# Optimization experiments

Measured on AMD Instinct MI355X. Metric: run time of the kernel, lower is better.

The kernel has to match this reference:

```python
import jax, jax.numpy as jnp
import numpy as np

# --- quantization helpers (I-BERT-style symmetric quantization) ---

def _quant_int(x, scale, bit):
    # round(x/scale) clamped to signed `bit`-bit range (SymmetricQuantFunction)
    n = 2 ** (bit - 1) - 1
    return jnp.clip(jnp.round(x / scale), -n - 1, n)


def quant_linear(x, s_x, W, b, weight_bit=8):
    """QuantLinear: per-output-channel symmetric 8-bit weight quant, int GEMM, dequant.
    Returns (output, bias_scaling_factor[out_features])."""
    n = 2 ** (weight_bit - 1) - 1
    w_scale = jnp.maximum(jnp.max(jnp.abs(W), axis=1), 1e-8) / n          # (out,)
    w_int = _quant_int(W, w_scale[:, None], weight_bit)                   # int-valued (out,in)
    b_scale = w_scale * s_x                                               # (out,) broadcasts with scalar s_x
    b_int = jnp.round(b / b_scale)                                        # 32-bit bias, no clamp needed
    x_int = x / s_x                                                       # int-valued activations
    out_int = jnp.einsum('bsi,oi->bso', x_int, w_int) + b_int
    return out_int * b_scale, b_scale


def quant_act(x, bit):
    """QuantAct: per-tensor symmetric requantization to `bit` bits (dynamic min/max)."""
    n = 2 ** (bit - 1) - 1
    scale = jnp.maximum(jnp.max(jnp.abs(x)), 1e-8) / n                    # scalar
    x_int = _quant_int(x, scale, bit)
    return x_int * scale, scale


def int_gelu(x, s):
    """IntGELU (I-BERT): integer 2nd-order polynomial approximation of erf."""
    k = 1.4142
    c0, c1 = -0.2888, -1.769
    c2 = 1.0 / c0
    SHIFT = 14  # 'const' in the original code

    x_int = x / s
    se = s / k  # scaling factor fed to int_erf
    # --- int_erf ---
    b_int = jnp.floor(c1 / se)
    c_int = jnp.floor(c2 / se ** 2)
    sign = jnp.sign(x_int)
    abs_int = jnp.minimum(jnp.abs(x_int), -b_int)
    y_int = sign * ((abs_int + b_int) ** 2 + c_int)
    se2 = se ** 2 * c0
    y_int = jnp.floor(y_int / 2 ** SHIFT)
    se2 = se2 * 2 ** SHIFT
    # --- gelu = x * (erf/2 + 1/2) in integer form ---
    shift_int = jnp.floor(1.0 / se2)
    out_int = x_int * (y_int + shift_int)
    s_out = s * se2 / 2
    return out_int * s_out, s_out


def setup_inputs() -> dict:
    key = jax.random.key(0)
    k_x, k_w1, k_b1, k_w2, k_b2 = jax.random.split(key, 5)
    B, S, D, H = 8, 1024, 768, 3072
    x = jax.random.normal(k_x, (B, S, D), dtype=jnp.float32)
    act_scaling_factor = jnp.full((1,), 0.02, dtype=jnp.float32)
    # pre-quantize x onto its input grid (x arrives already quantized in the real pipeline)
    x = jnp.round(x / act_scaling_factor) * act_scaling_factor
    W1 = jax.random.normal(k_w1, (H, D), dtype=jnp.float32) * 0.02
    b1 = jax.random.normal(k_b1, (H,), dtype=jnp.float32) * 0.02
    W2 = jax.random.normal(k_w2, (D, H), dtype=jnp.float32) * 0.02
    b2 = jax.random.normal(k_b2, (D,), dtype=jnp.float32) * 0.02
    return {"x": x, "act_scaling_factor": act_scaling_factor,
            "W1": W1, "b1": b1, "W2": W2, "b2": b2}


def reference(x, act_scaling_factor, W1, b1, W2, b2):
    s = act_scaling_factor
    h, s = quant_linear(x, s, W1, b1)       # fc1: int8 GEMM + dequant
    h, s = quant_act(h, 8)                  # qact_gelu
    h, s = int_gelu(h, s)                   # IntGELU
    h, s = quant_act(h, 8)                  # qact1 (drop=0.0 -> identity)
    h, s = quant_linear(h, s, W2, b2)       # fc2
    h, s = quant_act(h, 16)                 # qact2 (16-bit)
    return h, s
```

## Files before the change

kernel.cpp:

```cpp
#include <hip/hip_runtime.h>

typedef _Float16 half8  __attribute__((ext_vector_type(8)));
typedef _Float16 half4v __attribute__((ext_vector_type(4)));
typedef float f32x4 __attribute__((ext_vector_type(4)));
typedef int int4v __attribute__((ext_vector_type(4)));

#define M_DIM 8192
#define D_DIM 768
#define H_DIM 3072

#define WS_WSCALE2   16
#define WS_BINT1     (WS_WSCALE2 + 768*4)
#define WS_BSCALE1   (WS_BINT1 + 3072*4)
#define WS_BINT2     (WS_BSCALE1 + 3072*4)
#define WS_BSCALE2   (WS_BINT2 + 768*4)
#define WS_XQ        34560UL
#define WS_WQ1       (WS_XQ  + (size_t)M_DIM*D_DIM*2)
#define WS_WQ2I      (WS_WQ1 + (size_t)H_DIM*D_DIM*2)
#define WS_H1        (WS_WQ2I + (size_t)D_DIM*H_DIM)
#define WS_Q2        WS_H1
#define WS_H2        (WS_H1 + (size_t)M_DIM*H_DIM)
#define WS_Q1        (WS_H1 + (size_t)M_DIM*H_DIM*4)

__device__ __forceinline__ void gl_lds16(const _Float16* g, _Float16* l) {
  __builtin_amdgcn_global_load_lds(
      (const __attribute__((address_space(1))) void*)g,
      (__attribute__((address_space(3))) void*)l, 16, 0, 0);
}
__device__ __forceinline__ void gl_lds16c(const char* g, char* l) {
  __builtin_amdgcn_global_load_lds(
      (const __attribute__((address_space(1))) void*)g,
      (__attribute__((address_space(3))) void*)l, 16, 0, 0);
}

struct GeluP { float scale1, bintg, cintg, shiftint, s_out; };

__device__ __forceinline__ GeluP gelu_params(float max1) {
  GeluP p;
  p.scale1 = fmaxf(max1, 1e-8f) / 127.0f;
  float se = p.scale1 / 1.4142f;
  p.bintg = floorf(-1.769f / se);
  p.cintg = floorf(((float)(1.0 / -0.2888)) / (se * se));
  float se2 = ((se * se) * -0.2888f) * 16384.0f;
  p.shiftint = floorf(1.0f / se2);
  p.s_out = (p.scale1 * se2) * 0.5f;
  return p;
}

__device__ __forceinline__ float gelu_val(const GeluP& p, float qf) {
  float sg = (qf > 0.f) ? 1.f : ((qf < 0.f) ? -1.f : 0.f);
  float aq = fminf(fabsf(qf), -p.bintg);
  float t = aq + p.bintg;
  float y = sg * (t * t + p.cintg);
  float yf = floorf(y * (1.0f / 16384.0f));
  return (qf * (yf + p.shiftint)) * p.s_out;
}

__global__ __launch_bounds__(256)
void k1_prep(const float* __restrict__ W1, const float* __restrict__ b1,
             const float* __restrict__ W2, const float* __restrict__ sxp,
             _Float16* __restrict__ wq1, char* __restrict__ wq2i,
             float* __restrict__ wscale2, float* __restrict__ bint1,
             float* __restrict__ bscale1, unsigned* __restrict__ wsu)
{
  if (blockIdx.x == 0 && threadIdx.x == 0) { wsu[0] = 0u; wsu[1] = 0u; wsu[2] = 0u; }
  int w = blockIdx.x * 4 + (threadIdx.x >> 6);
  int lane = threadIdx.x & 63;
  if (w < H_DIM) {
    const float* row = W1 + (size_t)w * D_DIM;
    f32x4 v[3]; float m = 0.f;
#pragma unroll
    for (int t = 0; t < 3; t++) {
      v[t] = *(const f32x4*)(row + t * 256 + lane * 4);
#pragma unroll
      for (int j = 0; j < 4; j++) m = fmaxf(m, fabsf(v[t][j]));
    }
#pragma unroll
    for (int off = 32; off >= 1; off >>= 1) m = fmaxf(m, __shfl_xor(m, off));
    float wsc = fmaxf(m, 1e-8f) / 127.0f;
    _Float16* orow = wq1 + (size_t)w * D_DIM;
#pragma unroll
    for (int t = 0; t < 3; t++) {
      half4v h;
#pragma unroll
      for (int j = 0; j < 4; j++) {
        float q = fminf(fmaxf(rintf(v[t][j] / wsc), -128.f), 127.f);
        h[j] = (_Float16)q;
      }
      *(half4v*)(orow + t * 256 + lane * 4) = h;
    }
    if (lane == 0) {
      float bs = wsc * sxp[0];
      bint1[w] = rintf(b1[w] / bs);
      bscale1[w] = bs;
    }
  } else {
    int o = w - H_DIM;
    const float* row = W2 + (size_t)o * H_DIM;
    f32x4 v[12]; float m = 0.f;
#pragma unroll
    for (int t = 0; t < 12; t++) {
      v[t] = *(const f32x4*)(row + t * 256 + lane * 4);
#pragma unroll
      for (int j = 0; j < 4; j++) m = fmaxf(m, fabsf(v[t][j]));
    }
#pragma unroll
    for (int off = 32; off >= 1; off >>= 1) m = fmaxf(m, __shfl_xor(m, off));
    float wsc = fmaxf(m, 1e-8f) / 127.0f;
    unsigned* orow = (unsigned*)(wq2i + (size_t)o * H_DIM);
#pragma unroll
    for (int t = 0; t < 12; t++) {
      unsigned pk = 0;
#pragma unroll
      for (int j = 0; j < 4; j++) {
        float q = fminf(fmaxf(rintf(v[t][j] / wsc), -128.f), 127.f);
        pk |= ((unsigned)(unsigned char)(char)(int)q) << (8 * j);
      }
      orow[t * 64 + lane] = pk;
    }
    if (lane == 0) wscale2[o] = wsc;
  }
}

__global__ __launch_bounds__(256)
void k2_quant_x(const float* __restrict__ x, const float* __restrict__ sxp,
                _Float16* __restrict__ xq, int n4)
{
  float sx = sxp[0];
  int stride = gridDim.x * blockDim.x;
  for (int i = blockIdx.x * blockDim.x + threadIdx.x; i < n4; i += stride) {
    f32x4 v = ((const f32x4*)x)[i];
    half4v h;
#pragma unroll
    for (int j = 0; j < 4; j++) h[j] = (_Float16)(v[j] / sx);
    ((half4v*)xq)[i] = h;
  }
}

#define F16_SLOT 8192

__global__ __launch_bounds__(256)
void gemm_f16_dp(const _Float16* __restrict__ A, const _Float16* __restrict__ B,
                 const float* __restrict__ bint, const float* __restrict__ bscale,
                 float* __restrict__ C, unsigned* __restrict__ maxw, int N, int K)
{
  __shared__ _Float16 lds[3 * F16_SLOT];
  __shared__ float wred[4];
  const int tid = threadIdx.x;
  const int wid = tid >> 6;
  const int lane = tid & 63;
  const int m0 = blockIdx.x * 128;
  const int n0 = blockIdx.y * 128;
  const int wm = wid >> 1;
  const int wn = wid & 1;

  const int sr = tid >> 2;
  const int sc = tid & 3;
  const int csw = sc ^ ((sr >> 1) & 3);
  const _Float16* pa0 = A + (size_t)(m0 + sr) * K + csw * 8;
  const _Float16* pa1 = A + (size_t)(m0 + 64 + sr) * K + csw * 8;
  const _Float16* pb0 = B + (size_t)(n0 + sr) * K + csw * 8;
  const _Float16* pb1 = B + (size_t)(n0 + 64 + sr) * K + csw * 8;

#define STAGE_F(t, s) do {                                                   \
    _Float16* const base = lds + (s) * F16_SLOT + wid * 512;                 \
    gl_lds16(pa0 + (size_t)(t) * 32, base);                                  \
    gl_lds16(pa1 + (size_t)(t) * 32, base + 2048);                           \
    gl_lds16(pb0 + (size_t)(t) * 32, base + 4096);                           \
    gl_lds16(pb1 + (size_t)(t) * 32, base + 6144);                           \
  } while (0)

  int aoff[4], boff[4];
  const int ks = lane >> 4;
#pragma unroll
  for (int f = 0; f < 4; f++) {
    int r = wm * 64 + f * 16 + (lane & 15);
    aoff[f] = r * 64 + ((ks ^ ((r >> 1) & 3)) * 16);
    int rn = wn * 64 + f * 16 + (lane & 15);
    boff[f] = 8192 + rn * 64 + ((ks ^ ((rn >> 1) & 3)) * 16);
  }

  f32x4 acc[4][4];
#pragma unroll
  for (int i = 0; i < 4; i++)
#pragma unroll
    for (int j = 0; j < 4; j++) acc[i][j] = (f32x4){0.f, 0.f, 0.f, 0.f};

  const int nt = K / 32;
  STAGE_F(0, 0);
  STAGE_F(1, 1);
  for (int t = 0; t < nt; ++t) {
    const int s = t % 3;
    if (t + 1 < nt) asm volatile("s_waitcnt vmcnt(4)" ::: "memory");
    else            asm volatile("s_waitcnt vmcnt(0)" ::: "memory");
    asm volatile("s_barrier" ::: "memory");
    if (t + 2 < nt) STAGE_F(t + 2, (t + 2) % 3);
    const char* sb = (const char*)(lds + s * F16_SLOT);
    half8 a[4], b01[2], b23[2];
#pragma unroll
    for (int f = 0; f < 4; f++) a[f] = *(const half8*)(sb + aoff[f]);
    b01[0] = *(const half8*)(sb + boff[0]);
    b01[1] = *(const half8*)(sb + boff[1]);
    __builtin_amdgcn_s_setprio(1);
#pragma unroll
    for (int i = 0; i < 4; i++)
#pragma unroll
      for (int j = 0; j < 2; j++)
        acc[i][j] = __builtin_amdgcn_mfma_f32_16x16x32_f16(a[i], b01[j], acc[i][j], 0, 0, 0);
    __builtin_amdgcn_s_setprio(0);
    b23[0] = *(const half8*)(sb + boff[2]);
    b23[1] = *(const half8*)(sb + boff[3]);
    __builtin_amdgcn_s_setprio(1);
#pragma unroll
    for (int i = 0; i < 4; i++)
#pragma unroll
      for (int j = 0; j < 2; j++)
        acc[i][j + 2] = __builtin_amdgcn_mfma_f32_16x16x32_f16(a[i], b23[j], acc[i][j + 2], 0, 0, 0);
    __builtin_amdgcn_s_setprio(0);
  }
#undef STAGE_F

  float tmax = 0.f;
  const int orow0 = m0 + wm * 64 + (lane >> 4) * 4;
  const int ocol0 = n0 + wn * 64 + (lane & 15);
#pragma unroll
  for (int j = 0; j < 4; j++) {
    const int col = ocol0 + j * 16;
    const float bi = bint[col];
    const float bs = bscale[col];
#pragma unroll
    for (int i = 0; i < 4; i++) {
#pragma unroll
      for (int e = 0; e < 4; e++) {
        const int rowm = orow0 + i * 16 + e;
        float v = (acc[i][j][e] + bi) * bs;
        C[(size_t)rowm * N + col] = v;
        tmax = fmaxf(tmax, fabsf(v));
      }
    }
  }
#pragma unroll
  for (int off = 32; off >= 1; off >>= 1) tmax = fmaxf(tmax, __shfl_xor(tmax, off));
  if (lane == 0) wred[wid] = tmax;
  __syncthreads();
  if (tid == 0) {
    float bm = fmaxf(fmaxf(wred[0], wred[1]), fmaxf(wred[2], wred[3]));
    atomicMax(maxw, __float_as_uint(bm));
  }
}

__global__ __launch_bounds__(256)
void k4_gelu(const float* __restrict__ h1, const unsigned* __restrict__ wsu,
             char* __restrict__ q1, unsigned* __restrict__ maxw, int n4)
{
  GeluP p = gelu_params(__uint_as_float(wsu[0]));
  float tmax = 0.f;
  int stride = gridDim.x * blockDim.x;
  for (int i = blockIdx.x * blockDim.x + threadIdx.x; i < n4; i += stride) {
    f32x4 h = ((const f32x4*)h1)[i];
    unsigned pack = 0;
#pragma unroll
    for (int j = 0; j < 4; j++) {
      float qf = fminf(fmaxf(rintf(h[j] / p.scale1), -128.f), 127.f);
      tmax = fmaxf(tmax, fabsf(gelu_val(p, qf)));
      pack |= ((unsigned)(unsigned char)(char)(int)qf) << (8 * j);
    }
    ((unsigned*)q1)[i] = pack;
  }
#pragma unroll
  for (int off = 32; off >= 1; off >>= 1) tmax = fmaxf(tmax, __shfl_xor(tmax, off));
  __shared__ float wred[4];
  int wid = threadIdx.x >> 6;
  if ((threadIdx.x & 63) == 0) wred[wid] = tmax;
  __syncthreads();
  if (threadIdx.x == 0) {
    float bm = fmaxf(fmaxf(wred[0], wred[1]), fmaxf(wred[2], wred[3]));
    atomicMax(maxw, __float_as_uint(bm));
  }
}

__global__ __launch_bounds__(256)
void k6_bias(const unsigned* __restrict__ wsu, const float* __restrict__ wscale2,
             const float* __restrict__ b2, float* __restrict__ bint2,
             float* __restrict__ bscale2)
{
  float scale2 = fmaxf(__uint_as_float(wsu[1]), 1e-8f) / 127.0f;
  for (int o = threadIdx.x; o < D_DIM; o += 256) {
    float bs = wscale2[o] * scale2;
    bint2[o] = rintf(b2[o] / bs);
    bscale2[o] = bs;
  }
}

__global__ __launch_bounds__(256)
void k5_q2(const char* __restrict__ q1, const unsigned* __restrict__ wsu,
           char* __restrict__ q2, int n16)
{
  GeluP p = gelu_params(__uint_as_float(wsu[0]));
  float scale2 = fmaxf(__uint_as_float(wsu[1]), 1e-8f) / 127.0f;
  int stride = gridDim.x * blockDim.x;
  for (int i = blockIdx.x * blockDim.x + threadIdx.x; i < n16; i += stride) {
    uint4 pk = ((const uint4*)q1)[i];
    uint4 o;
    unsigned* pw[4] = {&o.x, &o.y, &o.z, &o.w};
    unsigned pr[4] = {pk.x, pk.y, pk.z, pk.w};
#pragma unroll
    for (int w = 0; w < 4; w++) {
      unsigned acc = 0;
#pragma unroll
      for (int j = 0; j < 4; j++) {
        float qf = (float)(int)(signed char)(pr[w] >> (8 * j));
        float g = gelu_val(p, qf);
        float q2f = fminf(fmaxf(rintf(g / scale2), -128.f), 127.f);
        acc |= ((unsigned)(unsigned char)(char)(int)q2f) << (8 * j);
      }
      *pw[w] = acc;
    }
    ((uint4*)q2)[i] = o;
  }
}

#define I8_SLOT 12288

__global__ __launch_bounds__(256)
void gemm_i8_dp(const char* __restrict__ A, const char* __restrict__ B,
                const float* __restrict__ bint, const float* __restrict__ bscale,
                float* __restrict__ C, unsigned* __restrict__ maxw, int N, int K)
{
  __shared__ char lds[3 * I8_SLOT];
  __shared__ float wred[4];
  const int tid = threadIdx.x;
  const int wid = tid >> 6;
  const int lane = tid & 63;
  const int m0 = blockIdx.x * 64;
  const int n0 = blockIdx.y * 128;
  const int wm = wid >> 1;
  const int wn = wid & 1;

  const int sr = tid >> 2;
  const int sc = tid & 3;
  const int csw = sc ^ ((sr >> 1) & 3);
  const char* pa  = A + (size_t)(m0 + sr) * K + csw * 16;
  const char* pb0 = B + (size_t)(n0 + sr) * K + csw * 16;
  const char* pb1 = B + (size_t)(n0 + 64 + sr) * K + csw * 16;

#define STAGE_I(t, s) do {                                                   \
    char* const base = lds + (s) * I8_SLOT + wid * 1024;                     \
    gl_lds16c(pa  + (size_t)(t) * 64, base);                                 \
    gl_lds16c(pb0 + (size_t)(t) * 64, base + 4096);                          \
    gl_lds16c(pb1 + (size_t)(t) * 64, base + 8192);                          \
  } while (0)

  int aoff[2], boff[4];
  const int ks = lane >> 4;
#pragma unroll
  for (int f = 0; f < 2; f++) {
    int r = wm * 32 + f * 16 + (lane & 15);
    aoff[f] = r * 64 + ((ks ^ ((r >> 1) & 3)) * 16);
  }
#pragma unroll
  for (int f = 0; f < 4; f++) {
    int rn = wn * 64 + f * 16 + (lane & 15);
    boff[f] = 4096 + rn * 64 + ((ks ^ ((rn >> 1) & 3)) * 16);
  }

  int4v acc[2][4];
#pragma unroll
  for (int i = 0; i < 2; i++)
#pragma unroll
    for (int j = 0; j < 4; j++) acc[i][j] = (int4v){0, 0, 0, 0};

  const int nt = K / 64;
  STAGE_I(0, 0);
  STAGE_I(1, 1);
  for (int t = 0; t < nt; ++t) {
    const int s = t % 3;
    if (t + 1 < nt) asm volatile("s_waitcnt vmcnt(3)" ::: "memory");
    else            asm volatile("s_waitcnt vmcnt(0)" ::: "memory");
    asm volatile("s_barrier" ::: "memory");
    if (t + 2 < nt) STAGE_I(t + 2, (t + 2) % 3);
    const char* sb = lds + s * I8_SLOT;
    int4v a[2], b01[2], b23[2];
#pragma unroll
    for (int f = 0; f < 2; f++) a[f] = *(const int4v*)(sb + aoff[f]);
    b01[0] = *(const int4v*)(sb + boff[0]);
    b01[1] = *(const int4v*)(sb + boff[1]);
    __builtin_amdgcn_s_setprio(1);
#pragma unroll
    for (int i = 0; i < 2; i++)
#pragma unroll
      for (int j = 0; j < 2; j++)
        acc[i][j] = __builtin_amdgcn_mfma_i32_16x16x64_i8(a[i], b01[j], acc[i][j], 0, 0, 0);
    __builtin_amdgcn_s_setprio(0);
    b23[0] = *(const int4v*)(sb + boff[2]);
    b23[1] = *(const int4v*)(sb + boff[3]);
    __builtin_amdgcn_s_setprio(1);
#pragma unroll
    for (int i = 0; i < 2; i++)
#pragma unroll
      for (int j = 0; j < 2; j++)
        acc[i][j + 2] = __builtin_amdgcn_mfma_i32_16x16x64_i8(a[i], b23[j], acc[i][j + 2], 0, 0, 0);
    __builtin_amdgcn_s_setprio(0);
  }
#undef STAGE_I

  float tmax = 0.f;
  const int orow0 = m0 + wm * 32 + (lane >> 4) * 4;
  const int ocol0 = n0 + wn * 64 + (lane & 15);
#pragma unroll
  for (int j = 0; j < 4; j++) {
    const int col = ocol0 + j * 16;
    const float bi = bint[col];
    const float bs = bscale[col];
#pragma unroll
    for (int i = 0; i < 2; i++) {
#pragma unroll
      for (int e = 0; e < 4; e++) {
        const int rowm = orow0 + i * 16 + e;
        float v = ((float)acc[i][j][e] + bi) * bs;
        C[(size_t)rowm * N + col] = v;
        tmax = fmaxf(tmax, fabsf(v));
      }
    }
  }
#pragma unroll
  for (int off = 32; off >= 1; off >>= 1) tmax = fmaxf(tmax, __shfl_xor(tmax, off));
  if (lane == 0) wred[wid] = tmax;
  __syncthreads();
  if (tid == 0) {
    float bm = fmaxf(fmaxf(wred[0], wred[1]), fmaxf(wred[2], wred[3]));
    atomicMax(maxw, __float_as_uint(bm));
  }
}

__global__ __launch_bounds__(256)
void k7_final(const float* __restrict__ h2, const unsigned* __restrict__ wsu,
              float* __restrict__ out, int n4, int ntot)
{
  float scale16 = fmaxf(__uint_as_float(wsu[2]), 1e-8f) / 32767.0f;
  int stride = gridDim.x * blockDim.x;
  for (int i = blockIdx.x * blockDim.x + threadIdx.x; i < n4; i += stride) {
    f32x4 v = ((const f32x4*)h2)[i];
    f32x4 o;
#pragma unroll
    for (int j = 0; j < 4; j++) {
      float q = fminf(fmaxf(rintf(v[j] / scale16), -32768.f), 32767.f);
      o[j] = q * scale16;
    }
    ((f32x4*)out)[i] = o;
  }
  if (blockIdx.x == 0 && threadIdx.x == 0) out[ntot] = scale16;
}

extern "C" void kernel_launch(void* const* d_in, const int* in_sizes, int n_in,
                              void* d_out, int out_size, void* d_ws, size_t ws_size,
                              hipStream_t stream)
{
  (void)in_sizes; (void)n_in; (void)out_size; (void)ws_size;
  const float* x  = (const float*)d_in[0];
  const float* sx = (const float*)d_in[1];
  const float* W1 = (const float*)d_in[2];
  const float* b1 = (const float*)d_in[3];
  const float* W2 = (const float*)d_in[4];
  const float* b2 = (const float*)d_in[5];
  float* out = (float*)d_out;
  char* ws = (char*)d_ws;

  unsigned* wsu   = (unsigned*)ws;
  float* wscale2  = (float*)(ws + WS_WSCALE2);
  float* bint1    = (float*)(ws + WS_BINT1);
  float* bscale1  = (float*)(ws + WS_BSCALE1);
  float* bint2    = (float*)(ws + WS_BINT2);
  float* bscale2  = (float*)(ws + WS_BSCALE2);
  _Float16* xq    = (_Float16*)(ws + WS_XQ);
  _Float16* wq1   = (_Float16*)(ws + WS_WQ1);
  char* wq2i      = (char*)(ws + WS_WQ2I);
  float* h1       = (float*)(ws + WS_H1);
  char* q2        = (char*)(ws + WS_Q2);
  float* h2       = (float*)(ws + WS_H2);
  char* q1        = (char*)(ws + WS_Q1);

  k1_prep<<<dim3(960), dim3(256), 0, stream>>>(W1, b1, W2, sx, wq1, wq2i, wscale2, bint1, bscale1, wsu);
  k2_quant_x<<<dim3(2048), dim3(256), 0, stream>>>(x, sx, xq, (M_DIM * D_DIM) / 4);
  gemm_f16_dp<<<dim3(64, 24), dim3(256), 0, stream>>>(xq, wq1, bint1, bscale1, h1, wsu + 0, H_DIM, D_DIM);
  k4_gelu<<<dim3(2048), dim3(256), 0, stream>>>(h1, wsu, q1, wsu + 1, (M_DIM * H_DIM) / 4);
  k6_bias<<<dim3(1), dim3(256), 0, stream>>>(wsu, wscale2, b2, bint2, bscale2);
  k5_q2<<<dim3(2048), dim3(256), 0, stream>>>(q1, wsu, q2, (M_DIM * H_DIM) / 16);
  gemm_i8_dp<<<dim3(128, 6), dim3(256), 0, stream>>>(q2, wq2i, bint2, bscale2, h2, wsu + 2, D_DIM, H_DIM);
  k7_final<<<dim3(2048), dim3(256), 0, stream>>>(h2, wsu, out, (M_DIM * D_DIM) / 4, M_DIM * D_DIM);
}
```

Before: 196.1 us.

## Rewrite fc1 GEMM as 256x256 8-phase pipeline and fuse prep kernels

The fc1 fp16 GEMM moves from 128x128 tiles with 4 waves and a 3-slot ring to 256x256 tiles with 8 waves. It uses a double-buffered 128 KB LDS layout with K=64 stages and an eight-phase schedule that interleaves global-to-LDS loads with MFMA groups. The goal is more data reuse per tile and better overlap of loads with math. Separately, the x-quantization kernel is merged into the weight-prep kernel, and the single-block fc2 bias kernel is folded into the int8 GEMM epilogue, which removes two launches. The large tile halves the grid and needs a lot of LDS and registers, so occupancy and tail effects are a risk.

```diff
diff --git a/kernel.cpp b/kernel.cpp
--- a/kernel.cpp
+++ b/kernel.cpp
@@ -12,8 +12,6 @@
 #define WS_WSCALE2   16
 #define WS_BINT1     (WS_WSCALE2 + 768*4)
 #define WS_BSCALE1   (WS_BINT1 + 3072*4)
-#define WS_BINT2     (WS_BSCALE1 + 3072*4)
-#define WS_BSCALE2   (WS_BINT2 + 768*4)
 #define WS_XQ        34560UL
 #define WS_WQ1       (WS_XQ  + (size_t)M_DIM*D_DIM*2)
 #define WS_WQ2I      (WS_WQ1 + (size_t)H_DIM*D_DIM*2)
@@ -31,6 +29,10 @@
   __builtin_amdgcn_global_load_lds(
       (const __attribute__((address_space(1))) void*)g,
       (__attribute__((address_space(3))) void*)l, 16, 0, 0);
+}
+__device__ __forceinline__ void vmw4or0(bool four) {
+  if (four) asm volatile("s_waitcnt vmcnt(4)" ::: "memory");
+  else      asm volatile("s_waitcnt vmcnt(0)" ::: "memory");
 }
 
 struct GeluP { float scale1, bintg, cintg, shiftint, s_out; };
@@ -57,183 +59,193 @@
 }
 
 __global__ __launch_bounds__(256)
-void k1_prep(const float* __restrict__ W1, const float* __restrict__ b1,
-             const float* __restrict__ W2, const float* __restrict__ sxp,
-             _Float16* __restrict__ wq1, char* __restrict__ wq2i,
-             float* __restrict__ wscale2, float* __restrict__ bint1,
-             float* __restrict__ bscale1, unsigned* __restrict__ wsu)
+void k12_prep(const float* __restrict__ W1, const float* __restrict__ b1,
+              const float* __restrict__ W2, const float* __restrict__ x,
+              const float* __restrict__ sxp,
+              _Float16* __restrict__ wq1, char* __restrict__ wq2i,
+              float* __restrict__ wscale2, float* __restrict__ bint1,
+              float* __restrict__ bscale1, _Float16* __restrict__ xq,
+              unsigned* __restrict__ wsu)
 {
   if (blockIdx.x == 0 && threadIdx.x == 0) { wsu[0] = 0u; wsu[1] = 0u; wsu[2] = 0u; }
-  int w = blockIdx.x * 4 + (threadIdx.x >> 6);
-  int lane = threadIdx.x & 63;
-  if (w < H_DIM) {
-    const float* row = W1 + (size_t)w * D_DIM;
-    f32x4 v[3]; float m = 0.f;
-#pragma unroll
-    for (int t = 0; t < 3; t++) {
-      v[t] = *(const f32x4*)(row + t * 256 + lane * 4);
-#pragma unroll
-      for (int j = 0; j < 4; j++) m = fmaxf(m, fabsf(v[t][j]));
-    }
-#pragma unroll
-    for (int off = 32; off >= 1; off >>= 1) m = fmaxf(m, __shfl_xor(m, off));
-    float wsc = fmaxf(m, 1e-8f) / 127.0f;
-    _Float16* orow = wq1 + (size_t)w * D_DIM;
-#pragma unroll
-    for (int t = 0; t < 3; t++) {
+  if (blockIdx.x < 960) {
+    int w = blockIdx.x * 4 + (threadIdx.x >> 6);
+    int lane = threadIdx.x & 63;
+    if (w < H_DIM) {
+      const float* row = W1 + (size_t)w * D_DIM;
+      f32x4 v[3]; float m = 0.f;
+#pragma unroll
+      for (int t = 0; t < 3; t++) {
+        v[t] = *(const f32x4*)(row + t * 256 + lane * 4);
+#pragma unroll
+        for (int j = 0; j < 4; j++) m = fmaxf(m, fabsf(v[t][j]));
+      }
+#pragma unroll
+      for (int off = 32; off >= 1; off >>= 1) m = fmaxf(m, __shfl_xor(m, off));
+      float wsc = fmaxf(m, 1e-8f) / 127.0f;
+      _Float16* orow = wq1 + (size_t)w * D_DIM;
+#pragma unroll
+      for (int t = 0; t < 3; t++) {
+        half4v h;
+#pragma unroll
+        for (int j = 0; j < 4; j++) {
+          float q = fminf(fmaxf(rintf(v[t][j] / wsc), -128.f), 127.f);
+          h[j] = (_Float16)q;
+        }
+        *(half4v*)(orow + t * 256 + lane * 4) = h;
+      }
+      if (lane == 0) {
+        float bs = wsc * sxp[0];
+        bint1[w] = rintf(b1[w] / bs);
+        bscale1[w] = bs;
+      }
+    } else {
+      int o = w - H_DIM;
+      const float* row = W2 + (size_t)o * H_DIM;
+      f32x4 v[12]; float m = 0.f;
+#pragma unroll
+      for (int t = 0; t < 12; t++) {
+        v[t] = *(const f32x4*)(row + t * 256 + lane * 4);
+#pragma unroll
+        for (int j = 0; j < 4; j++) m = fmaxf(m, fabsf(v[t][j]));
+      }
+#pragma unroll
+      for (int off = 32; off >= 1; off >>= 1) m = fmaxf(m, __shfl_xor(m, off));
+      float wsc = fmaxf(m, 1e-8f) / 127.0f;
+      unsigned* orow = (unsigned*)(wq2i + (size_t)o * H_DIM);
+#pragma unroll
+      for (int t = 0; t < 12; t++) {
+        unsigned pk = 0;
+#pragma unroll
+        for (int j = 0; j < 4; j++) {
+          float q = fminf(fmaxf(rintf(v[t][j] / wsc), -128.f), 127.f);
+          pk |= ((unsigned)(unsigned char)(char)(int)q) << (8 * j);
+        }
+        orow[t * 64 + lane] = pk;
+      }
+      if (lane == 0) wscale2[o] = wsc;
+    }
+  } else {
+    float sx = sxp[0];
+    const int n4 = (M_DIM * D_DIM) / 4;
+    const int stride = 1024 * 256;
+    for (int i = (blockIdx.x - 960) * 256 + threadIdx.x; i < n4; i += stride) {
+      f32x4 v = ((const f32x4*)x)[i];
       half4v h;
 #pragma unroll
-      for (int j = 0; j < 4; j++) {
-        float q = fminf(fmaxf(rintf(v[t][j] / wsc), -128.f), 127.f);
-        h[j] = (_Float16)q;
-      }
-      *(half4v*)(orow + t * 256 + lane * 4) = h;
-    }
-    if (lane == 0) {
-      float bs = wsc * sxp[0];
-      bint1[w] = rintf(b1[w] / bs);
-      bscale1[w] = bs;
-    }
-  } else {
-    int o = w - H_DIM;
-    const float* row = W2 + (size_t)o * H_DIM;
-    f32x4 v[12]; float m = 0.f;
-#pragma unroll
-    for (int t = 0; t < 12; t++) {
-      v[t] = *(const f32x4*)(row + t * 256 + lane * 4);
-#pragma unroll
-      for (int j = 0; j < 4; j++) m = fmaxf(m, fabsf(v[t][j]));
-    }
-#pragma unroll
-    for (int off = 32; off >= 1; off >>= 1) m = fmaxf(m, __shfl_xor(m, off));
-    float wsc = fmaxf(m, 1e-8f) / 127.0f;
-    unsigned* orow = (unsigned*)(wq2i + (size_t)o * H_DIM);
-#pragma unroll
-    for (int t = 0; t < 12; t++) {
-      unsigned pk = 0;
-#pragma unroll
-      for (int j = 0; j < 4; j++) {
-        float q = fminf(fmaxf(rintf(v[t][j] / wsc), -128.f), 127.f);
-        pk |= ((unsigned)(unsigned char)(char)(int)q) << (8 * j);
-      }
-      orow[t * 64 + lane] = pk;
-    }
-    if (lane == 0) wscale2[o] = wsc;
-  }
-}
-
-__global__ __launch_bounds__(256)
-void k2_quant_x(const float* __restrict__ x, const float* __restrict__ sxp,
-                _Float16* __restrict__ xq, int n4)
-{
-  float sx = sxp[0];
-  int stride = gridDim.x * blockDim.x;
-  for (int i = blockIdx.x * blockDim.x + threadIdx.x; i < n4; i += stride) {
-    f32x4 v = ((const f32x4*)x)[i];
-    half4v h;
-#pragma unroll
-    for (int j = 0; j < 4; j++) h[j] = (_Float16)(v[j] / sx);
-    ((half4v*)xq)[i] = h;
-  }
-}
-
-#define F16_SLOT 8192
-
-__global__ __launch_bounds__(256)
-void gemm_f16_dp(const _Float16* __restrict__ A, const _Float16* __restrict__ B,
+      for (int j = 0; j < 4; j++) h[j] = (_Float16)(v[j] / sx);
+      ((half4v*)xq)[i] = h;
+    }
+  }
+}
+
+#define STAGE_A8(buf, h, t) do {                                              \
+    const _Float16* _s = pa + (size_t)(h) * 128 * K + (size_t)(t) * 64;       \
+    _Float16* _d = lds + (buf) * 32768 + (h) * 8192 + w * 512;                \
+    gl_lds16(_s, _d);                                                         \
+    gl_lds16(_s + (size_t)64 * K, _d + 4096);                                 \
+  } while (0)
+#define STAGE_B8(buf, h, t) do {                                              \
+    const _Float16* _s = pb + (size_t)(h) * 128 * K + (size_t)(t) * 64;       \
+    _Float16* _d = lds + (buf) * 32768 + 16384 + (h) * 8192 + w * 512;        \
+    gl_lds16(_s, _d);                                                         \
+    gl_lds16(_s + (size_t)64 * K, _d + 4096);                                 \
+  } while (0)
+#define PHASE8(buf, qq, DOB, STMT, VMSTMT) do {                               \
+    const char* _sb = (const char*)lds + (buf) * 65536;                       \
+    half8 a00 = *(const half8*)(_sb + abase + (2*(qq)) * 2048 + c0);          \
+    half8 a01 = *(const half8*)(_sb + abase + (2*(qq)) * 2048 + c1);          \
+    half8 a10 = *(const half8*)(_sb + abase + (2*(qq)+1) * 2048 + c0);        \
+    half8 a11 = *(const half8*)(_sb + abase + (2*(qq)+1) * 2048 + c1);        \
+    if (DOB) {                                                                \
+      _Pragma("unroll")                                                       \
+      for (int nf = 0; nf < 4; nf++) {                                        \
+        bfr[nf][0] = *(const half8*)(_sb + bbase + nf * 2048 + c0);           \
+        bfr[nf][1] = *(const half8*)(_sb + bbase + nf * 2048 + c1);           \
+      }                                                                       \
+    }                                                                         \
+    STMT;                                                                     \
+    VMSTMT;                                                                   \
+    asm volatile("s_barrier" ::: "memory");                                   \
+    __builtin_amdgcn_s_setprio(1);                                            \
+    _Pragma("unroll")                                                         \
+    for (int nf = 0; nf < 4; nf++) {                                          \
+      acc[2*(qq)][nf]   = __builtin_amdgcn_mfma_f32_16x16x32_f16(a00, bfr[nf][0], acc[2*(qq)][nf],   0, 0, 0); \
+      acc[2*(qq)][nf]   = __builtin_amdgcn_mfma_f32_16x16x32_f16(a01, bfr[nf][1], acc[2*(qq)][nf],   0, 0, 0); \
+      acc[2*(qq)+1][nf] = __builtin_amdgcn_mfma_f32_16x16x32_f16(a10, bfr[nf][0], acc[2*(qq)+1][nf], 0, 0, 0); \
+      acc[2*(qq)+1][nf] = __builtin_amdgcn_mfma_f32_16x16x32_f16(a11, bfr[nf][1], acc[2*(qq)+1][nf], 0, 0, 0); \
+    }                                                                         \
+    __builtin_amdgcn_s_setprio(0);                                            \
+    asm volatile("s_barrier" ::: "memory");                                   \
+  } while (0)
+
+__global__ __launch_bounds__(512, 2)
+void gemm_f16_8p(const _Float16* __restrict__ A, const _Float16* __restrict__ B,
                  const float* __restrict__ bint, const float* __restrict__ bscale,
                  float* __restrict__ C, unsigned* __restrict__ maxw, int N, int K)
 {
-  __shared__ _Float16 lds[3 * F16_SLOT];
-  __shared__ float wred[4];
+  __shared__ _Float16 lds[65536];
+  __shared__ float wred[8];
   const int tid = threadIdx.x;
-  const int wid = tid >> 6;
-  const int lane = tid & 63;
-  const int m0 = blockIdx.x * 128;
-  const int n0 = blockIdx.y * 128;
-  const int wm = wid >> 1;
-  const int wn = wid & 1;
-
-  const int sr = tid >> 2;
-  const int sc = tid & 3;
-  const int csw = sc ^ ((sr >> 1) & 3);
-  const _Float16* pa0 = A + (size_t)(m0 + sr) * K + csw * 8;
-  const _Float16* pa1 = A + (size_t)(m0 + 64 + sr) * K + csw * 8;
-  const _Float16* pb0 = B + (size_t)(n0 + sr) * K + csw * 8;
-  const _Float16* pb1 = B + (size_t)(n0 + 64 + sr) * K + csw * 8;
-
-#define STAGE_F(t, s) do {                                                   \
-    _Float16* const base = lds + (s) * F16_SLOT + wid * 512;                 \
-    gl_lds16(pa0 + (size_t)(t) * 32, base);                                  \
-    gl_lds16(pa1 + (size_t)(t) * 32, base + 2048);                           \
-    gl_lds16(pb0 + (size_t)(t) * 32, base + 4096);                           \
-    gl_lds16(pb1 + (size_t)(t) * 32, base + 6144);                           \
-  } while (0)
-
-  int aoff[4], boff[4];
-  const int ks = lane >> 4;
-#pragma unroll
-  for (int f = 0; f < 4; f++) {
-    int r = wm * 64 + f * 16 + (lane & 15);
-    aoff[f] = r * 64 + ((ks ^ ((r >> 1) & 3)) * 16);
-    int rn = wn * 64 + f * 16 + (lane & 15);
-    boff[f] = 8192 + rn * 64 + ((ks ^ ((rn >> 1) & 3)) * 16);
-  }
-
-  f32x4 acc[4][4];
-#pragma unroll
-  for (int i = 0; i < 4; i++)
+  const int w = tid >> 6;
+  const int l = tid & 63;
+  const int m0 = blockIdx.x * 256;
+  const int n0 = blockIdx.y * 256;
+  const int wm = w >> 2;
+  const int wn = w & 3;
+
+  const int srow = 8 * w + (l >> 3);
+  const int swc  = (l & 7) ^ (l >> 3);
+  const _Float16* pa = A + (size_t)(m0 + srow) * K + swc * 8;
+  const _Float16* pb = B + (size_t)(n0 + srow) * K + swc * 8;
+
+  const int c0 = (((l >> 4)) ^ (l & 7)) * 16;
+  const int c1 = ((4 + (l >> 4)) ^ (l & 7)) * 16;
+  const int abase = (wm * 128 + (l & 15)) * 128;
+  const int bbase = 32768 + (wn * 64 + (l & 15)) * 128;
+
+  f32x4 acc[8][4];
+#pragma unroll
+  for (int i = 0; i < 8; i++)
 #pragma unroll
     for (int j = 0; j < 4; j++) acc[i][j] = (f32x4){0.f, 0.f, 0.f, 0.f};
-
-  const int nt = K / 32;
-  STAGE_F(0, 0);
-  STAGE_F(1, 1);
-  for (int t = 0; t < nt; ++t) {
-    const int s = t % 3;
-    if (t + 1 < nt) asm volatile("s_waitcnt vmcnt(4)" ::: "memory");
-    else            asm volatile("s_waitcnt vmcnt(0)" ::: "memory");
-    asm volatile("s_barrier" ::: "memory");
-    if (t + 2 < nt) STAGE_F(t + 2, (t + 2) % 3);
-    const char* sb = (const char*)(lds + s * F16_SLOT);
-    half8 a[4], b01[2], b23[2];
-#pragma unroll
-    for (int f = 0; f < 4; f++) a[f] = *(const half8*)(sb + aoff[f]);
-    b01[0] = *(const half8*)(sb + boff[0]);
-    b01[1] = *(const half8*)(sb + boff[1]);
-    __builtin_amdgcn_s_setprio(1);
-#pragma unroll
-    for (int i = 0; i < 4; i++)
-#pragma unroll
-      for (int j = 0; j < 2; j++)
-        acc[i][j] = __builtin_amdgcn_mfma_f32_16x16x32_f16(a[i], b01[j], acc[i][j], 0, 0, 0);
-    __builtin_amdgcn_s_setprio(0);
-    b23[0] = *(const half8*)(sb + boff[2]);
-    b23[1] = *(const half8*)(sb + boff[3]);
-    __builtin_amdgcn_s_setprio(1);
-#pragma unroll
-    for (int i = 0; i < 4; i++)
-#pragma unroll
-      for (int j = 0; j < 2; j++)
-        acc[i][j + 2] = __builtin_amdgcn_mfma_f32_16x16x32_f16(a[i], b23[j], acc[i][j + 2], 0, 0, 0);
-    __builtin_amdgcn_s_setprio(0);
-  }
-#undef STAGE_F
+  half8 bfr[4][2];
+
+  const int nt = K >> 6;
+  STAGE_B8(0, 0, 0); STAGE_B8(0, 1, 0);
+  STAGE_A8(0, 0, 0); STAGE_A8(0, 1, 0);
+  STAGE_B8(1, 0, 1); STAGE_B8(1, 1, 1);
+  asm volatile("s_waitcnt vmcnt(4)" ::: "memory");
+  asm volatile("s_barrier" ::: "memory");
+
+  for (int i = 0; i < (nt >> 1); ++i) {
+    const int t0 = 2 * i, t1 = 2 * i + 1;
+    const bool g = (t0 + 2 < nt);
+    PHASE8(0, 0, true,  STAGE_A8(1, 0, t1), );
+    PHASE8(0, 1, false, STAGE_A8(1, 1, t1), );
+    PHASE8(0, 2, false, if (g) STAGE_B8(0, 0, t0 + 2), );
+    PHASE8(0, 3, false, if (g) STAGE_B8(0, 1, t0 + 2), vmw4or0(g));
+    PHASE8(1, 0, true,  if (g) STAGE_A8(0, 0, t0 + 2), );
+    PHASE8(1, 1, false, if (g) STAGE_A8(0, 1, t0 + 2), );
+    PHASE8(1, 2, false, if (g) STAGE_B8(1, 0, t1 + 2), );
+    PHASE8(1, 3, false, if (g) STAGE_B8(1, 1, t1 + 2),
+           if (g) asm volatile("s_waitcnt vmcnt(4)" ::: "memory"));
+  }
 
   float tmax = 0.f;
-  const int orow0 = m0 + wm * 64 + (lane >> 4) * 4;
-  const int ocol0 = n0 + wn * 64 + (lane & 15);
-#pragma unroll
-  for (int j = 0; j < 4; j++) {
-    const int col = ocol0 + j * 16;
+  const int orow0 = m0 + wm * 128 + (l >> 4) * 4;
+  const int ocol0 = n0 + wn * 64 + (l & 15);
+#pragma unroll
+  for (int nf = 0; nf < 4; nf++) {
+    const int col = ocol0 + nf * 16;
     const float bi = bint[col];
     const float bs = bscale[col];
 #pragma unroll
-    for (int i = 0; i < 4; i++) {
+    for (int mi = 0; mi < 8; mi++) {
 #pragma unroll
       for (int e = 0; e < 4; e++) {
-        const int rowm = orow0 + i * 16 + e;
-        float v = (acc[i][j][e] + bi) * bs;
+        const int rowm = orow0 + mi * 16 + e;
+        float v = (acc[mi][nf][e] + bi) * bs;
         C[(size_t)rowm * N + col] = v;
         tmax = fmaxf(tmax, fabsf(v));
       }
@@ -241,10 +253,12 @@
   }
 #pragma unroll
   for (int off = 32; off >= 1; off >>= 1) tmax = fmaxf(tmax, __shfl_xor(tmax, off));
-  if (lane == 0) wred[wid] = tmax;
+  if (l == 0) wred[w] = tmax;
   __syncthreads();
   if (tid == 0) {
-    float bm = fmaxf(fmaxf(wred[0], wred[1]), fmaxf(wred[2], wred[3]));
+    float bm = 0.f;
+#pragma unroll
+    for (int i = 0; i < 8; i++) bm = fmaxf(bm, wred[i]);
     atomicMax(maxw, __float_as_uint(bm));
   }
 }
@@ -280,19 +294,6 @@
 }
 
 __global__ __launch_bounds__(256)
-void k6_bias(const unsigned* __restrict__ wsu, const float* __restrict__ wscale2,
-             const float* __restrict__ b2, float* __restrict__ bint2,
-             float* __restrict__ bscale2)
-{
-  float scale2 = fmaxf(__uint_as_float(wsu[1]), 1e-8f) / 127.0f;
-  for (int o = threadIdx.x; o < D_DIM; o += 256) {
-    float bs = wscale2[o] * scale2;
-    bint2[o] = rintf(b2[o] / bs);
-    bscale2[o] = bs;
-  }
-}
-
-__global__ __launch_bounds__(256)
 void k5_q2(const char* __restrict__ q1, const unsigned* __restrict__ wsu,
            char* __restrict__ q2, int n16)
 {
@@ -324,8 +325,9 @@
 
 __global__ __launch_bounds__(256)
 void gemm_i8_dp(const char* __restrict__ A, const char* __restrict__ B,
-                const float* __restrict__ bint, const float* __restrict__ bscale,
-                float* __restrict__ C, unsigned* __restrict__ maxw, int N, int K)
+                const unsigned* __restrict__ wsu, const float* __restrict__ wscale2,
+                const float* __restrict__ b2, float* __restrict__ C,
+                unsigned* __restrict__ maxw, int N, int K)
 {
   __shared__ char lds[3 * I8_SLOT];
   __shared__ float wred[4];
@@ -336,6 +338,7 @@
   const int n0 = blockIdx.y * 128;
   const int wm = wid >> 1;
   const int wn = wid & 1;
+  const float scale2 = fmaxf(__uint_as_float(wsu[1]), 1e-8f) / 127.0f;
 
   const int sr = tid >> 2;
   const int sc = tid & 3;
@@ -410,8 +413,8 @@
 #pragma unroll
   for (int j = 0; j < 4; j++) {
     const int col = ocol0 + j * 16;
-    const float bi = bint[col];
-    const float bs = bscale[col];
+    const float bs = wscale2[col] * scale2;
+    const float bi = rintf(b2[col] / bs);
 #pragma unroll
     for (int i = 0; i < 2; i++) {
 #pragma unroll
@@ -470,8 +473,6 @@
   float* wscale2  = (float*)(ws + WS_WSCALE2);
   float* bint1    = (float*)(ws + WS_BINT1);
   float* bscale1  = (float*)(ws + WS_BSCALE1);
-  float* bint2    = (float*)(ws + WS_BINT2);
-  float* bscale2  = (float*)(ws + WS_BSCALE2);
   _Float16* xq    = (_Float16*)(ws + WS_XQ);
   _Float16* wq1   = (_Float16*)(ws + WS_WQ1);
   char* wq2i      = (char*)(ws + WS_WQ2I);
@@ -480,12 +481,11 @@
   float* h2       = (float*)(ws + WS_H2);
   char* q1        = (char*)(ws + WS_Q1);
 
-  k1_prep<<<dim3(960), dim3(256), 0, stream>>>(W1, b1, W2, sx, wq1, wq2i, wscale2, bint1, bscale1, wsu);
-  k2_quant_x<<<dim3(2048), dim3(256), 0, stream>>>(x, sx, xq, (M_DIM * D_DIM) / 4);
-  gemm_f16_dp<<<dim3(64, 24), dim3(256), 0, stream>>>(xq, wq1, bint1, bscale1, h1, wsu + 0, H_DIM, D_DIM);
+  k12_prep<<<dim3(1984), dim3(256), 0, stream>>>(W1, b1, W2, x, sx, wq1, wq2i,
+                                                 wscale2, bint1, bscale1, xq, wsu);
+  gemm_f16_8p<<<dim3(32, 12), dim3(512), 0, stream>>>(xq, wq1, bint1, bscale1, h1, wsu + 0, H_DIM, D_DIM);
   k4_gelu<<<dim3(2048), dim3(256), 0, stream>>>(h1, wsu, q1, wsu + 1, (M_DIM * H_DIM) / 4);
-  k6_bias<<<dim3(1), dim3(256), 0, stream>>>(wsu, wscale2, b2, bint2, bscale2);
   k5_q2<<<dim3(2048), dim3(256), 0, stream>>>(q1, wsu, q2, (M_DIM * H_DIM) / 16);
-  gemm_i8_dp<<<dim3(128, 6), dim3(256), 0, stream>>>(q2, wq2i, bint2, bscale2, h2, wsu + 2, D_DIM, H_DIM);
+  gemm_i8_dp<<<dim3(128, 6), dim3(256), 0, stream>>>(q2, wq2i, wsu, wscale2, b2, h2, wsu + 2, D_DIM, H_DIM);
   k7_final<<<dim3(2048), dim3(256), 0, stream>>>(h2, wsu, out, (M_DIM * D_DIM) / 4, M_DIM * D_DIM);
 }
```

After: 187.0 us. 4.6% less time.
